# Performance work log

Measured on AMD Instinct MI355X. Metric: run time of the kernel, lower is better.

Reference implementation:

```python
import jax, jax.numpy as jnp
import numpy as np

H = 16  # num_heads
KEEP_PROB = 0.9


def setup_inputs() -> dict:
    key = jax.random.key(0)
    ks = jax.random.split(key, 12)
    B, S, D = 2, 2048, 1024
    x = jax.random.normal(ks[0], (B, S, D), dtype=jnp.float32)
    # random sparsity mask over full score tensor [B, H, S_q, S_k]; True = keep
    keep_mask = jax.random.uniform(ks[1], (B, H, S, S)) > (1.0 - KEEP_PROB)
    init = 0.02
    Wq = jax.random.normal(ks[2], (D, D), dtype=jnp.float32) * init
    bq = jax.random.normal(ks[3], (D,), dtype=jnp.float32) * init
    Wk = jax.random.normal(ks[4], (D, D), dtype=jnp.float32) * init
    bk = jax.random.normal(ks[5], (D,), dtype=jnp.float32) * init
    Wv = jax.random.normal(ks[6], (D, D), dtype=jnp.float32) * init
    bv = jax.random.normal(ks[7], (D,), dtype=jnp.float32) * init
    Wo = jax.random.normal(ks[8], (D, D), dtype=jnp.float32) * init
    bo = jax.random.normal(ks[9], (D,), dtype=jnp.float32) * init
    return {"x": x, "keep_mask": keep_mask, "Wq": Wq, "bq": bq, "Wk": Wk,
            "bk": bk, "Wv": Wv, "bv": bv, "Wo": Wo, "bo": bo}


def reference(x, keep_mask, Wq, bq, Wk, bk, Wv, bv, Wo, bo):
    B, S, D = x.shape
    hd = D // H
    scale = hd ** (-0.5)
    # torch nn.Linear: y = x @ W.T + b
    def proj(W, b):
        return (x @ W.T + b).reshape(B, S, H, hd).transpose(0, 2, 1, 3)  # [B,H,S,hd]
    Q = proj(Wq, bq)
    K = proj(Wk, bk)
    V = proj(Wv, bv)
    scores = jnp.einsum('bhqd,bhkd->bhqk', Q, K) * scale  # [B,H,S,S]
    neg_inf = jnp.float32(-jnp.inf)
    scores = jnp.where(keep_mask, scores, neg_inf)
    attn = jax.nn.softmax(scores, axis=-1)
    attn = jnp.nan_to_num(attn, nan=0.0)  # rows fully masked -> 0 (matches torch)
    # dropout_rate = 0.0 (eval-mode deterministic baseline) -> identity
    ctx = jnp.einsum('bhqk,bhkd->bhqd', attn, V)  # [B,H,S,hd]
    ctx = ctx.transpose(0, 2, 1, 3).reshape(B, S, D)  # [B,S,D]
    return ctx @ Wo.T + bo
```

## Files before the change

### kernel.cpp

```cpp
#include <hip/hip_runtime.h>
#include <cstdint>
#include <cstddef>

constexpr int S_ = 2048;
constexpr int D_ = 1024;

typedef __attribute__((ext_vector_type(8))) short bf16x8;
typedef __attribute__((ext_vector_type(4))) float f32x4;

typedef __attribute__((address_space(1))) const unsigned int as1_uint;
typedef __attribute__((address_space(3))) unsigned int as3_uint;
#define ASYNC_CP16(g, l) \
  __builtin_amdgcn_global_load_lds((as1_uint*)(g), (as3_uint*)(l), 16, 0, 0)

__device__ __forceinline__ unsigned short f2b(float f) {
  unsigned int u = __float_as_uint(f);
  u += 0x7fffu + ((u >> 16) & 1u);
  return (unsigned short)(u >> 16);
}

__global__ void cvt_x(const float* __restrict__ src, unsigned short* __restrict__ dst) {
  int i = (blockIdx.x * 256 + threadIdx.x) * 4;
  float4 v = *reinterpret_cast<const float4*>(src + i);
  ushort4 o;
  o.x = f2b(v.x); o.y = f2b(v.y); o.z = f2b(v.z); o.w = f2b(v.w);
  *reinterpret_cast<ushort4*>(dst + i) = o;
}

__global__ void cvt_w(const float* __restrict__ w0, const float* __restrict__ w1,
                      const float* __restrict__ w2, const float* __restrict__ w3,
                      unsigned short* __restrict__ dst) {
  int i = (blockIdx.x * 256 + threadIdx.x) * 4;
  int which = i >> 20;
  const float* s = (which == 0) ? w0 : (which == 1) ? w1 : (which == 2) ? w2 : w3;
  float4 v = *reinterpret_cast<const float4*>(s + (i & 1048575));
  ushort4 o;
  o.x = f2b(v.x); o.y = f2b(v.y); o.z = f2b(v.z); o.w = f2b(v.w);
  *reinterpret_cast<ushort4*>(dst + i) = o;
}

__global__ void pack_bias(const float* __restrict__ b0, const float* __restrict__ b1,
                          const float* __restrict__ b2, float* __restrict__ dst) {
  const float* s = (blockIdx.x == 0) ? b0 : (blockIdx.x == 1) ? b1 : b2;
  dst[blockIdx.x * 1024 + threadIdx.x] = s[threadIdx.x];
}

template <int MODE>
__global__ __launch_bounds__(256) void gemm_bt(
    const unsigned short* __restrict__ A,
    const unsigned short* __restrict__ Bm,
    const float* __restrict__ bias,
    void* __restrict__ out) {
  constexpr int K = 1024;
  __shared__ __align__(16) unsigned short sA[128 * 64];
  __shared__ __align__(16) unsigned short sB[128 * 64];
  const int tid = threadIdx.x;
  const int w = tid >> 6, lane = tid & 63;
  const int l15 = lane & 15, quad = lane >> 4, l7 = lane & 7;
  const int m0 = blockIdx.y * 128, n0 = blockIdx.x * 128;
  const int wm = (w >> 1) * 64, wn = (w & 1) * 64;

  const int lr = lane >> 3;
  const int lc = l7 ^ lr;
  const unsigned short* ga = A + (size_t)(m0 + w * 32 + lr) * K + lc * 8;
  const unsigned short* gb = Bm + (size_t)(n0 + w * 32 + lr) * K + lc * 8;
  unsigned short* la = sA + w * 32 * 64;
  unsigned short* lb = sB + w * 32 * 64;

  f32x4 acc[4][4] = {};

  for (int kt = 0; kt < K; kt += 64) {
    __syncthreads();
#pragma unroll
    for (int c = 0; c < 4; ++c) {
      ASYNC_CP16(ga + c * 8 * K + kt, la + c * 8 * 64);
      ASYNC_CP16(gb + c * 8 * K + kt, lb + c * 8 * 64);
    }
    __syncthreads();
#pragma unroll
    for (int s = 0; s < 2; ++s) {
      bf16x8 af[4], bfr[4];
#pragma unroll
      for (int mt = 0; mt < 4; ++mt)
        af[mt] = *reinterpret_cast<const bf16x8*>(
            sA + (wm + mt * 16 + l15) * 64 + ((s * 4 + quad) ^ (l15 & 7)) * 8);
#pragma unroll
      for (int nt = 0; nt < 4; ++nt)
        bfr[nt] = *reinterpret_cast<const bf16x8*>(
            sB + (wn + nt * 16 + l15) * 64 + ((s * 4 + quad) ^ (l15 & 7)) * 8);
#pragma unroll
      for (int mt = 0; mt < 4; ++mt)
#pragma unroll
        for (int nt = 0; nt < 4; ++nt)
          acc[mt][nt] = __builtin_amdgcn_mfma_f32_16x16x32_bf16(af[mt], bfr[nt], acc[mt][nt], 0, 0, 0);
    }
  }

#pragma unroll
  for (int mt = 0; mt < 4; ++mt) {
#pragma unroll
    for (int nt = 0; nt < 4; ++nt) {
      int col = n0 + wn + nt * 16 + l15;
      float bv = bias[col];
#pragma unroll
      for (int rr = 0; rr < 4; ++rr) {
        int row = m0 + wm + mt * 16 + quad * 4 + rr;
        float v = acc[mt][nt][rr] + bv;
        if (MODE == 0) {
          ((float*)out)[(size_t)row * 1024 + col] = v;
        } else {
          int which = col >> 10, rem = col & 1023;
          int h = rem >> 6, d = rem & 63;
          int b = row >> 11, s = row & 2047;
          ((unsigned short*)out)[(size_t)which * 4194304 +
                                 (((size_t)(b * 16 + h) * 2048 + s) * 64 + d)] = f2b(v);
        }
      }
    }
  }
}

__global__ __launch_bounds__(256) void attn_kernel(
    const unsigned short* __restrict__ Q,
    const unsigned short* __restrict__ K,
    const unsigned short* __restrict__ V,
    const int* __restrict__ mask,
    unsigned short* __restrict__ ctx) {
  constexpr int LDP = 136;
  __shared__ __align__(16) unsigned short sK[128 * 64];
  __shared__ __align__(16) unsigned short sVT[64 * LDP];
  __shared__ __align__(16) unsigned short sP[4 * 16 * LDP];
  const int tid = threadIdx.x;
  const int w = tid >> 6, lane = tid & 63;
  const int l15 = lane & 15, quad = lane >> 4, l7 = lane & 7;
  const int bh = blockIdx.y;
  const int b = bh >> 4, h = bh & 15;
  const unsigned short* Qp = Q + (size_t)bh * S_ * 64;
  const unsigned short* Kp = K + (size_t)bh * S_ * 64;
  const unsigned short* Vp = V + (size_t)bh * S_ * 64;
  const int* mp = mask + (size_t)bh * S_ * S_;
  const int qw = blockIdx.x * 64 + w * 16;

  bf16x8 aq[2];
  aq[0] = *reinterpret_cast<const bf16x8*>(Qp + (size_t)(qw + l15) * 64 + quad * 8);
  aq[1] = *reinterpret_cast<const bf16x8*>(Qp + (size_t)(qw + l15) * 64 + 32 + quad * 8);

  float l_run[4] = {0.f, 0.f, 0.f, 0.f};
  f32x4 o[4] = {};

  const int lr = lane >> 3;
  const int lc = l7 ^ lr;
  const unsigned short* gk = Kp + (size_t)(w * 32 + lr) * 64 + lc * 8;
  unsigned short* lk = sK + w * 32 * 64;
  const int vr = tid >> 1;
  const int vc = (tid & 1) * 32;

  for (int kt = 0; kt < S_; kt += 128) {
    __syncthreads();
#pragma unroll
    for (int c = 0; c < 4; ++c)
      ASYNC_CP16(gk + (size_t)(kt + c * 8) * 64, lk + c * 8 * 64);
    {
      const int4* vg = reinterpret_cast<const int4*>(Vp + (size_t)(kt + vr) * 64 + vc);
      int4 v0 = vg[0], v1 = vg[1], v2 = vg[2], v3 = vg[3];
      const unsigned short* p0 = reinterpret_cast<const unsigned short*>(&v0);
      const unsigned short* p1 = reinterpret_cast<const unsigned short*>(&v1);
      const unsigned short* p2 = reinterpret_cast<const unsigned short*>(&v2);
      const unsigned short* p3 = reinterpret_cast<const unsigned short*>(&v3);
#pragma unroll
      for (int j = 0; j < 8; ++j) {
        sVT[(vc + j) * LDP + vr] = p0[j];
        sVT[(vc + 8 + j) * LDP + vr] = p1[j];
        sVT[(vc + 16 + j) * LDP + vr] = p2[j];
        sVT[(vc + 24 + j) * LDP + vr] = p3[j];
      }
    }
    __syncthreads();

#pragma unroll
    for (int nt = 0; nt < 8; ++nt) {
      f32x4 sacc = {0.f, 0.f, 0.f, 0.f};
#pragma unroll
      for (int s = 0; s < 2; ++s) {
        bf16x8 bk = *reinterpret_cast<const bf16x8*>(
            sK + (nt * 16 + l15) * 64 + ((s * 4 + quad) ^ (l15 & 7)) * 8);
        sacc = __builtin_amdgcn_mfma_f32_16x16x32_bf16(aq[s], bk, sacc, 0, 0, 0);
      }
      const int kcol = kt + nt * 16 + l15;
      const int* mrow = mp + (size_t)(qw + quad * 4) * S_ + kcol;
#pragma unroll
      for (int rr = 0; rr < 4; ++rr) {
        int keep = mrow[(size_t)rr * S_];
        float p = keep ? __expf(fmaf(sacc[rr], 0.125f, -8.0f)) : 0.f;
        l_run[rr] += p;
        sP[w * 16 * LDP + (quad * 4 + rr) * LDP + nt * 16 + l15] = f2b(p);
      }
    }

#pragma unroll
    for (int s4 = 0; s4 < 4; ++s4) {
      bf16x8 ap = *reinterpret_cast<const bf16x8*>(
          sP + w * 16 * LDP + l15 * LDP + s4 * 32 + quad * 8);
#pragma unroll
      for (int dt = 0; dt < 4; ++dt) {
        bf16x8 bv = *reinterpret_cast<const bf16x8*>(
            sVT + (dt * 16 + l15) * LDP + s4 * 32 + quad * 8);
        o[dt] = __builtin_amdgcn_mfma_f32_16x16x32_bf16(ap, bv, o[dt], 0, 0, 0);
      }
    }
  }

#pragma unroll
  for (int d = 1; d < 16; d <<= 1)
#pragma unroll
    for (int rr = 0; rr < 4; ++rr)
      l_run[rr] += __shfl_xor(l_run[rr], d, 64);

  float inv[4];
#pragma unroll
  for (int rr = 0; rr < 4; ++rr) inv[rr] = (l_run[rr] > 0.f) ? (1.0f / l_run[rr]) : 0.f;
#pragma unroll
  for (int dt = 0; dt < 4; ++dt)
#pragma unroll
    for (int rr = 0; rr < 4; ++rr) {
      int qrow = qw + quad * 4 + rr;
      ctx[((size_t)b * S_ + qrow) * D_ + h * 64 + dt * 16 + l15] = f2b(o[dt][rr] * inv[rr]);
    }
}

extern "C" void kernel_launch(void* const* d_in, const int* in_sizes, int n_in,
                              void* d_out, int out_size, void* d_ws, size_t ws_size,
                              hipStream_t stream) {
  const float* x    = (const float*)d_in[0];
  const int*   mask = (const int*)d_in[1];
  const float* Wq   = (const float*)d_in[2];
  const float* bq   = (const float*)d_in[3];
  const float* Wk   = (const float*)d_in[4];
  const float* bk   = (const float*)d_in[5];
  const float* Wv   = (const float*)d_in[6];
  const float* bv   = (const float*)d_in[7];
  const float* Wo   = (const float*)d_in[8];
  const float* bo   = (const float*)d_in[9];
  float* out = (float*)d_out;

  char* ws = (char*)d_ws;
  const size_t MB = 1048576;
  unsigned short* xb   = (unsigned short*)(ws);
  unsigned short* Wcat = (unsigned short*)(ws + 8 * MB);
  unsigned short* Qw   = (unsigned short*)(ws + 16 * MB);
  unsigned short* Cw   = (unsigned short*)(ws + 40 * MB);
  float*          bcat = (float*)(ws + 48 * MB);

  unsigned short* Kw = Qw + 4194304;
  unsigned short* Vw = Kw + 4194304;

  cvt_x<<<4096, 256, 0, stream>>>(x, xb);
  cvt_w<<<4096, 256, 0, stream>>>(Wq, Wk, Wv, Wo, Wcat);
  pack_bias<<<3, 1024, 0, stream>>>(bq, bk, bv, bcat);

  gemm_bt<1><<<dim3(24, 32), 256, 0, stream>>>(xb, Wcat, bcat, Qw);
  attn_kernel<<<dim3(32, 32), 256, 0, stream>>>(Qw, Kw, Vw, mask, Cw);
  gemm_bt<0><<<dim3(8, 32), 256, 0, stream>>>(Cw, Wcat + 3 * 1048576, bo, out);
}
```

Before: 879.6 us.

## Write V transposed from QKV GEMM and swap MFMA operands in attention

```diff
diff --git a/kernel.cpp b/kernel.cpp
--- a/kernel.cpp
+++ b/kernel.cpp
@@ -17,6 +17,12 @@
   unsigned int u = __float_as_uint(f);
   u += 0x7fffu + ((u >> 16) & 1u);
   return (unsigned short)(u >> 16);
+}
+
+__device__ __forceinline__ unsigned int pk2(float a, float b) {
+  unsigned int ua = __float_as_uint(a) + 0x8000u;
+  unsigned int ub = __float_as_uint(b) + 0x8000u;
+  return __builtin_amdgcn_perm(ub, ua, 0x07060302u);
 }
 
 __global__ void cvt_x(const float* __restrict__ src, unsigned short* __restrict__ dst) {
@@ -50,7 +56,7 @@
     const unsigned short* __restrict__ A,
     const unsigned short* __restrict__ Bm,
     const float* __restrict__ bias,
-    void* __restrict__ out) {
+    void* __restrict__ out, void* __restrict__ out2) {
   constexpr int K = 1024;
   __shared__ __align__(16) unsigned short sA[128 * 64];
   __shared__ __align__(16) unsigned short sB[128 * 64];
@@ -102,18 +108,33 @@
     for (int nt = 0; nt < 4; ++nt) {
       int col = n0 + wn + nt * 16 + l15;
       float bv = bias[col];
-#pragma unroll
-      for (int rr = 0; rr < 4; ++rr) {
-        int row = m0 + wm + mt * 16 + quad * 4 + rr;
-        float v = acc[mt][nt][rr] + bv;
-        if (MODE == 0) {
-          ((float*)out)[(size_t)row * 1024 + col] = v;
+      int row0 = m0 + wm + mt * 16 + quad * 4;
+      float v0 = acc[mt][nt][0] + bv, v1 = acc[mt][nt][1] + bv;
+      float v2 = acc[mt][nt][2] + bv, v3 = acc[mt][nt][3] + bv;
+      if (MODE == 0) {
+        float* op = (float*)out;
+        op[(size_t)(row0 + 0) * 1024 + col] = v0;
+        op[(size_t)(row0 + 1) * 1024 + col] = v1;
+        op[(size_t)(row0 + 2) * 1024 + col] = v2;
+        op[(size_t)(row0 + 3) * 1024 + col] = v3;
+      } else {
+        int which = col >> 10, rem = col & 1023;
+        int h = rem >> 6, d = rem & 63;
+        int b = row0 >> 11, s0 = row0 & 2047;
+        int bh = b * 16 + h;
+        if (which == 2) {
+          uint2 pv;
+          pv.x = pk2(v0, v1);
+          pv.y = pk2(v2, v3);
+          *reinterpret_cast<uint2*>((unsigned short*)out2 +
+                                    ((size_t)bh * 64 + d) * 2048 + s0) = pv;
         } else {
-          int which = col >> 10, rem = col & 1023;
-          int h = rem >> 6, d = rem & 63;
-          int b = row >> 11, s = row & 2047;
-          ((unsigned short*)out)[(size_t)which * 4194304 +
-                                 (((size_t)(b * 16 + h) * 2048 + s) * 64 + d)] = f2b(v);
+          unsigned short* op = (unsigned short*)out + (size_t)which * 4194304 +
+                               (((size_t)bh * 2048 + s0) * 64 + d);
+          op[0 * 64] = f2b(v0);
+          op[1 * 64] = f2b(v1);
+          op[2 * 64] = f2b(v2);
+          op[3 * 64] = f2b(v3);
         }
       }
     }
@@ -123,12 +144,12 @@
 __global__ __launch_bounds__(256) void attn_kernel(
     const unsigned short* __restrict__ Q,
     const unsigned short* __restrict__ K,
-    const unsigned short* __restrict__ V,
+    const unsigned short* __restrict__ Vt,
     const int* __restrict__ mask,
     unsigned short* __restrict__ ctx) {
   constexpr int LDP = 136;
   __shared__ __align__(16) unsigned short sK[128 * 64];
-  __shared__ __align__(16) unsigned short sVT[64 * LDP];
+  __shared__ __align__(16) unsigned short sVT[64 * 128];
   __shared__ __align__(16) unsigned short sP[4 * 16 * LDP];
   const int tid = threadIdx.x;
   const int w = tid >> 6, lane = tid & 63;
@@ -137,7 +158,7 @@
   const int b = bh >> 4, h = bh & 15;
   const unsigned short* Qp = Q + (size_t)bh * S_ * 64;
   const unsigned short* Kp = K + (size_t)bh * S_ * 64;
-  const unsigned short* Vp = V + (size_t)bh * S_ * 64;
+  const unsigned short* Vp = Vt + (size_t)bh * 64 * S_;
   const int* mp = mask + (size_t)bh * S_ * S_;
   const int qw = blockIdx.x * 64 + w * 16;
 
@@ -145,35 +166,26 @@
   aq[0] = *reinterpret_cast<const bf16x8*>(Qp + (size_t)(qw + l15) * 64 + quad * 8);
   aq[1] = *reinterpret_cast<const bf16x8*>(Qp + (size_t)(qw + l15) * 64 + 32 + quad * 8);
 
-  float l_run[4] = {0.f, 0.f, 0.f, 0.f};
+  float l_run = 0.f;
   f32x4 o[4] = {};
 
   const int lr = lane >> 3;
-  const int lc = l7 ^ lr;
-  const unsigned short* gk = Kp + (size_t)(w * 32 + lr) * 64 + lc * 8;
+  const int lcK = l7 ^ lr;
+  const unsigned short* gk = Kp + (size_t)(w * 32 + lr) * 64 + lcK * 8;
   unsigned short* lk = sK + w * 32 * 64;
-  const int vr = tid >> 1;
-  const int vc = (tid & 1) * 32;
+  const int vrow_base = w * 16 + quad;
+  unsigned short* sPw = sP + w * 16 * LDP;
 
   for (int kt = 0; kt < S_; kt += 128) {
     __syncthreads();
 #pragma unroll
     for (int c = 0; c < 4; ++c)
       ASYNC_CP16(gk + (size_t)(kt + c * 8) * 64, lk + c * 8 * 64);
-    {
-      const int4* vg = reinterpret_cast<const int4*>(Vp + (size_t)(kt + vr) * 64 + vc);
-      int4 v0 = vg[0], v1 = vg[1], v2 = vg[2], v3 = vg[3];
-      const unsigned short* p0 = reinterpret_cast<const unsigned short*>(&v0);
-      const unsigned short* p1 = reinterpret_cast<const unsigned short*>(&v1);
-      const unsigned short* p2 = reinterpret_cast<const unsigned short*>(&v2);
-      const unsigned short* p3 = reinterpret_cast<const unsigned short*>(&v3);
-#pragma unroll
-      for (int j = 0; j < 8; ++j) {
-        sVT[(vc + j) * LDP + vr] = p0[j];
-        sVT[(vc + 8 + j) * LDP + vr] = p1[j];
-        sVT[(vc + 16 + j) * LDP + vr] = p2[j];
-        sVT[(vc + 24 + j) * LDP + vr] = p3[j];
-      }
+#pragma unroll
+    for (int c = 0; c < 4; ++c) {
+      int vrow = vrow_base + c * 4;
+      ASYNC_CP16(Vp + (size_t)vrow * S_ + kt + ((l15 ^ (vrow & 7)) * 8),
+                 sVT + (w * 16 + c * 4) * 128);
     }
     __syncthreads();
 
@@ -182,50 +194,47 @@
       f32x4 sacc = {0.f, 0.f, 0.f, 0.f};
 #pragma unroll
       for (int s = 0; s < 2; ++s) {
-        bf16x8 bk = *reinterpret_cast<const bf16x8*>(
+        bf16x8 ak = *reinterpret_cast<const bf16x8*>(
             sK + (nt * 16 + l15) * 64 + ((s * 4 + quad) ^ (l15 & 7)) * 8);
-        sacc = __builtin_amdgcn_mfma_f32_16x16x32_bf16(aq[s], bk, sacc, 0, 0, 0);
+        sacc = __builtin_amdgcn_mfma_f32_16x16x32_bf16(ak, aq[s], sacc, 0, 0, 0);
       }
-      const int kcol = kt + nt * 16 + l15;
-      const int* mrow = mp + (size_t)(qw + quad * 4) * S_ + kcol;
-#pragma unroll
-      for (int rr = 0; rr < 4; ++rr) {
-        int keep = mrow[(size_t)rr * S_];
-        float p = keep ? __expf(fmaf(sacc[rr], 0.125f, -8.0f)) : 0.f;
-        l_run[rr] += p;
-        sP[w * 16 * LDP + (quad * 4 + rr) * LDP + nt * 16 + l15] = f2b(p);
+      const int4 mv = *reinterpret_cast<const int4*>(
+          mp + (size_t)(qw + l15) * S_ + kt + nt * 16 + quad * 4);
+      float p0 = mv.x ? __expf(fmaf(sacc[0], 0.125f, -8.0f)) : 0.f;
+      float p1 = mv.y ? __expf(fmaf(sacc[1], 0.125f, -8.0f)) : 0.f;
+      float p2 = mv.z ? __expf(fmaf(sacc[2], 0.125f, -8.0f)) : 0.f;
+      float p3 = mv.w ? __expf(fmaf(sacc[3], 0.125f, -8.0f)) : 0.f;
+      l_run += (p0 + p1) + (p2 + p3);
+      uint2 pw;
+      pw.x = pk2(p0, p1);
+      pw.y = pk2(p2, p3);
+      *reinterpret_cast<uint2*>(sPw + l15 * LDP + nt * 16 + quad * 4) = pw;
+    }
+
+#pragma unroll
+    for (int c = 0; c < 4; ++c) {
+      bf16x8 bp = *reinterpret_cast<const bf16x8*>(sPw + l15 * LDP + c * 32 + quad * 8);
+#pragma unroll
+      for (int dt = 0; dt < 4; ++dt) {
+        bf16x8 av = *reinterpret_cast<const bf16x8*>(
+            sVT + (dt * 16 + l15) * 128 + (((c * 4 + quad) ^ (l15 & 7)) * 8));
+        o[dt] = __builtin_amdgcn_mfma_f32_16x16x32_bf16(av, bp, o[dt], 0, 0, 0);
       }
     }
-
-#pragma unroll
-    for (int s4 = 0; s4 < 4; ++s4) {
-      bf16x8 ap = *reinterpret_cast<const bf16x8*>(
-          sP + w * 16 * LDP + l15 * LDP + s4 * 32 + quad * 8);
-#pragma unroll
-      for (int dt = 0; dt < 4; ++dt) {
-        bf16x8 bv = *reinterpret_cast<const bf16x8*>(
-            sVT + (dt * 16 + l15) * LDP + s4 * 32 + quad * 8);
-        o[dt] = __builtin_amdgcn_mfma_f32_16x16x32_bf16(ap, bv, o[dt], 0, 0, 0);
-      }
-    }
-  }
-
-#pragma unroll
-  for (int d = 1; d < 16; d <<= 1)
-#pragma unroll
-    for (int rr = 0; rr < 4; ++rr)
-      l_run[rr] += __shfl_xor(l_run[rr], d, 64);
-
-  float inv[4];
-#pragma unroll
-  for (int rr = 0; rr < 4; ++rr) inv[rr] = (l_run[rr] > 0.f) ? (1.0f / l_run[rr]) : 0.f;
-#pragma unroll
-  for (int dt = 0; dt < 4; ++dt)
-#pragma unroll
-    for (int rr = 0; rr < 4; ++rr) {
-      int qrow = qw + quad * 4 + rr;
-      ctx[((size_t)b * S_ + qrow) * D_ + h * 64 + dt * 16 + l15] = f2b(o[dt][rr] * inv[rr]);
-    }
+  }
+
+  l_run += __shfl_xor(l_run, 16, 64);
+  l_run += __shfl_xor(l_run, 32, 64);
+  float invl = (l_run > 0.f) ? (1.0f / l_run) : 0.f;
+
+  unsigned short* cp = ctx + ((size_t)(b * 2048 + qw + l15)) * 1024 + h * 64 + quad * 4;
+#pragma unroll
+  for (int dt = 0; dt < 4; ++dt) {
+    uint2 ov;
+    ov.x = pk2(o[dt][0] * invl, o[dt][1] * invl);
+    ov.y = pk2(o[dt][2] * invl, o[dt][3] * invl);
+    *reinterpret_cast<uint2*>(cp + dt * 16) = ov;
+  }
 }
 
 extern "C" void kernel_launch(void* const* d_in, const int* in_sizes, int n_in,
@@ -248,17 +257,17 @@
   unsigned short* xb   = (unsigned short*)(ws);
   unsigned short* Wcat = (unsigned short*)(ws + 8 * MB);
   unsigned short* Qw   = (unsigned short*)(ws + 16 * MB);
+  unsigned short* Vt   = (unsigned short*)(ws + 32 * MB);
   unsigned short* Cw   = (unsigned short*)(ws + 40 * MB);
   float*          bcat = (float*)(ws + 48 * MB);
 
   unsigned short* Kw = Qw + 4194304;
-  unsigned short* Vw = Kw + 4194304;
 
   cvt_x<<<4096, 256, 0, stream>>>(x, xb);
   cvt_w<<<4096, 256, 0, stream>>>(Wq, Wk, Wv, Wo, Wcat);
   pack_bias<<<3, 1024, 0, stream>>>(bq, bk, bv, bcat);
 
-  gemm_bt<1><<<dim3(24, 32), 256, 0, stream>>>(xb, Wcat, bcat, Qw);
-  attn_kernel<<<dim3(32, 32), 256, 0, stream>>>(Qw, Kw, Vw, mask, Cw);
-  gemm_bt<0><<<dim3(8, 32), 256, 0, stream>>>(Cw, Wcat + 3 * 1048576, bo, out);
-}
+  gemm_bt<1><<<dim3(24, 32), 256, 0, stream>>>(xb, Wcat, bcat, Qw, Vt);
+  attn_kernel<<<dim3(32, 32), 256, 0, stream>>>(Qw, Kw, Vt, mask, Cw);
+  gemm_bt<0><<<dim3(8, 32), 256, 0, stream>>>(Cw, Wcat + 3 * 1048576, bo, out, nullptr);
+}
```

Result: no change. 894.1 us (+1.7%).
